# Kernel optimization log

Measured on AMD Instinct MI355X. Metric: run time of the kernel, lower is better.

Reference implementation:

```python
import jax, jax.numpy as jnp
import numpy as np

B, S, D, E, K = 4, 4096, 2048, 64, 2
LN_EPS = 1e-5
TEMP_EPS = 1e-6
Z_LOSS_COEF = 0.001
LB_COEF = 0.1


def setup_inputs() -> dict:
    key = jax.random.key(0)
    k1, k2 = jax.random.split(key)
    x = jax.random.normal(k1, (B, S, D), dtype=jnp.float32)
    # kaiming_normal fan_in (std = 1/sqrt(D)) scaled by 0.01, as in __init__
    W = jax.random.normal(k2, (E, D), dtype=jnp.float32) * jnp.float32(0.01 / np.sqrt(D))
    gamma = jnp.ones((E,), jnp.float32)   # LayerNorm weight
    beta = jnp.zeros((E,), jnp.float32)   # LayerNorm bias
    temperature = jnp.full((1,), 0.5, jnp.float32)
    return {"x": x, "W": W, "gamma": gamma, "beta": beta, "temperature": temperature}


def reference(x, W, gamma, beta, temperature):
    b, s, d = x.shape
    xf = x.reshape(-1, d)                                  # [N, D]
    logits = xf @ W.T                                      # [N, E]
    # LayerNorm over expert dim (biased variance, eps=1e-5, matches torch)
    mu = logits.mean(axis=-1, keepdims=True)
    var = jnp.mean(jnp.square(logits - mu), axis=-1, keepdims=True)
    logits = (logits - mu) * jax.lax.rsqrt(var + LN_EPS) * gamma + beta
    # temperature-scaled softmax
    routing_weights = jax.nn.softmax(logits / (temperature + TEMP_EPS), axis=-1)  # [N, E]
    # top-k + scatter into dense dispatch mask
    top_w, top_idx = jax.lax.top_k(routing_weights, K)     # [N, K]
    n = routing_weights.shape[0]
    dispatch = jnp.zeros_like(routing_weights).at[jnp.arange(n)[:, None], top_idx].set(top_w)
    dispatch = dispatch.reshape(b, s, E)                   # [B, S, E]
    # aux losses
    expert_load = dispatch.mean(axis=1)                    # [B, E]
    load_balance_loss = jnp.std(expert_load, ddof=1) / expert_load.mean() * 10.0
    router_z_loss = jnp.mean(jnp.square(logits))
    total_loss = ZLC * router_z_loss + LB_COEF * load_balance_loss if False else (
        Z_LOSS_COEF * router_z_loss + LB_COEF * load_balance_loss)
    return jax.lax.stop_gradient(routing_weights), dispatch, total_loss
```

## Files before the change

kernel.cpp:

```cpp
#include <hip/hip_runtime.h>
#include <hip/hip_bf16.h>
#include <float.h>
#include <math.h>

#define B_DIM 4
#define S_DIM 4096
#define D_DIM 2048
#define E_DIM 64
#define N_TOK 16384
#define TOKS 32
#define NBLK (N_TOK / TOKS)
#define NTHR 256
#define SLICES 4
#define DSLICE (D_DIM / SLICES)
#define KSTEPS2 16
#define GAP_THRESH 1e-3f
#define MAXFLAG 16

typedef __bf16 bf16x8_t __attribute__((ext_vector_type(8)));
typedef float f32x4_t __attribute__((ext_vector_type(4)));

union U8 { bf16x8_t v; unsigned short u[8]; };

__device__ __forceinline__ void split2(float f, unsigned short& h, unsigned short& l) {
    unsigned int u = __float_as_uint(f);
    h = (unsigned short)(u >> 16);
    float hf = __uint_as_float(u & 0xFFFF0000u);
    l = (unsigned short)(__float_as_uint(f - hf) >> 16);
}

typedef const __attribute__((address_space(1))) unsigned int* gas1_t;
typedef __attribute__((address_space(3))) unsigned int* las3_t;
__device__ __forceinline__ void gll16(const unsigned short* g, unsigned short* l) {
    __builtin_amdgcn_global_load_lds((gas1_t)(const void*)g, (las3_t)(void*)l, 16, 0, 0);
}

__global__ void wsplit(const float* __restrict__ W, unsigned short* __restrict__ wh,
                       unsigned short* __restrict__ wl, float* __restrict__ wshdr) {
    const int i = blockIdx.x * 256 + threadIdx.x;
    if (blockIdx.x == 0) { wshdr[threadIdx.x] = 0.f; wshdr[threadIdx.x + 256] = 0.f; }
    const int e    = i >> 8;
    const int k8   = i & 255;
    const int quad = k8 & 3;
    const int h    = (k8 >> 2) & 1;
    const int s    = (k8 >> 3) & 7;
    const int sl   = k8 >> 6;
    const int t    = e >> 4;
    const int l15  = e & 15;
    const int lane = quad * 16 + l15;
    const size_t f = ((size_t)((sl * 8 + s) * 2 + h) * 4 + t) * 64 + lane;
    float4 a = *(const float4*)(W + (size_t)e * D_DIM + k8 * 8);
    float4 b = *(const float4*)(W + (size_t)e * D_DIM + k8 * 8 + 4);
    ushort4 h0, l0, h1, l1;
    split2(a.x, h0.x, l0.x); split2(a.y, h0.y, l0.y);
    split2(a.z, h0.z, l0.z); split2(a.w, h0.w, l0.w);
    split2(b.x, h1.x, l1.x); split2(b.y, h1.y, l1.y);
    split2(b.z, h1.z, l1.z); split2(b.w, h1.w, l1.w);
    *(ushort4*)(wh + f * 8)     = h0;
    *(ushort4*)(wh + f * 8 + 4) = h1;
    *(ushort4*)(wl + f * 8)     = l0;
    *(ushort4*)(wl + f * 8 + 4) = l1;
}

__global__ __launch_bounds__(NTHR, 2) void router_main(
    const float* __restrict__ x, const float* __restrict__ W,
    const unsigned short* __restrict__ whg, const unsigned short* __restrict__ wlg,
    const float* __restrict__ gamma, const float* __restrict__ beta,
    const float* __restrict__ temperature,
    float* __restrict__ out_rw, float* __restrict__ out_dp,
    float* __restrict__ g_zsum, float* __restrict__ g_load)
{
    __shared__ __align__(16) unsigned char arena[65536];
    unsigned short* const bufH = (unsigned short*)arena;
    unsigned short* const bufL = (unsigned short*)(arena + 32768);
    float (* const part)[TOKS][E_DIM + 2] = (float (*)[TOKS][E_DIM + 2])arena;
    float (* const lgt)[E_DIM + 1] = (float (*)[E_DIM + 1])(arena + 33792);

    __shared__ float lgm[E_DIM], lbt[E_DIM], loadsum[E_DIM];
    __shared__ float smu[TOKS], srs[TOKS], sinv[TOKS];
    __shared__ int sel1[TOKS], sel2[TOKS];
    __shared__ int ftok[MAXFLAG], fcand[MAXFLAG][3];
    __shared__ int nflag;

    const int tid = threadIdx.x;
    const int tokBase = blockIdx.x * TOKS;
    const int lane = tid & 63;
    const int wv = tid >> 6;
    const int l15 = lane & 15;
    const int quad = lane >> 4;

    if (tid == 0) nflag = 0;
    if (tid < E_DIM) { lgm[tid] = gamma[tid]; lbt[tid] = beta[tid]; loadsum[tid] = 0.f; }

    const float* xp0 = x + (size_t)(tokBase + l15) * D_DIM      + wv * DSLICE + quad * 8;
    const float* xp1 = x + (size_t)(tokBase + 16 + l15) * D_DIM + wv * DSLICE + quad * 8;

    const unsigned short* hsrc0 = whg + (size_t)wv * 16 * 2048 + lane * 8;
    const unsigned short* lsrc0 = wlg + (size_t)wv * 16 * 2048 + lane * 8;
    unsigned short* const hdst0 = bufH + wv * 2 * 2048 + lane * 8;
    unsigned short* const ldst0 = bufL + wv * 2 * 2048 + lane * 8;

#define STAGE(S2, B) do {                                                   \
        const unsigned short* hs = hsrc0 + (size_t)(S2) * 2048;             \
        const unsigned short* ls = lsrc0 + (size_t)(S2) * 2048;             \
        unsigned short* hd = hdst0 + (B) * 2048;                            \
        unsigned short* ld = ldst0 + (B) * 2048;                            \
        gll16(hs,        hd);        gll16(ls,        ld);                  \
        gll16(hs +  512, hd +  512); gll16(ls +  512, ld +  512);           \
        gll16(hs + 1024, hd + 1024); gll16(ls + 1024, ld + 1024);           \
        gll16(hs + 1536, hd + 1536); gll16(ls + 1536, ld + 1536);           \
    } while (0)

    f32x4_t acc[2][4];
    #pragma unroll
    for (int m = 0; m < 2; ++m)
        #pragma unroll
        for (int t = 0; t < 4; ++t) acc[m][t] = (f32x4_t){0.f, 0.f, 0.f, 0.f};

    STAGE(0, 0);
    float4 xqA[4], xqB[4];
    xqA[0] = *(const float4*)(xp0);  xqA[1] = *(const float4*)(xp0 + 4);
    xqA[2] = *(const float4*)(xp1);  xqA[3] = *(const float4*)(xp1 + 4);
    asm volatile("s_waitcnt vmcnt(0)" ::: "memory");
    __builtin_amdgcn_sched_barrier(0);

    for (int s2 = 0; s2 < KSTEPS2; ++s2) {
        const int cur = s2 & 1;
        const bool more = (s2 + 1 < KSTEPS2);
        if (more) {
            STAGE(s2 + 1, cur ^ 1);
            const float* xg0 = xp0 + (s2 + 1) * 32;
            const float* xg1 = xp1 + (s2 + 1) * 32;
            xqB[0] = *(const float4*)(xg0);  xqB[1] = *(const float4*)(xg0 + 4);
            xqB[2] = *(const float4*)(xg1);  xqB[3] = *(const float4*)(xg1 + 4);
        }
        const unsigned short* hb = bufH + (wv * 2 + cur) * 2048;
        const unsigned short* lb = bufL + (wv * 2 + cur) * 2048;
        bf16x8_t bh[4], bl[4];
        #pragma unroll
        for (int t = 0; t < 4; ++t) {
            bh[t] = *(const bf16x8_t*)(hb + t * 512 + lane * 8);
            bl[t] = *(const bf16x8_t*)(lb + t * 512 + lane * 8);
        }
        #pragma unroll
        for (int m = 0; m < 2; ++m) {
            float tf[8] = {xqA[m*2].x, xqA[m*2].y, xqA[m*2].z, xqA[m*2].w,
                           xqA[m*2+1].x, xqA[m*2+1].y, xqA[m*2+1].z, xqA[m*2+1].w};
            U8 ah, al;
            #pragma unroll
            for (int k = 0; k < 8; ++k) split2(tf[k], ah.u[k], al.u[k]);
            #pragma unroll
            for (int t = 0; t < 4; ++t) {
                acc[m][t] = __builtin_amdgcn_mfma_f32_16x16x32_bf16(ah.v, bh[t], acc[m][t], 0, 0, 0);
                acc[m][t] = __builtin_amdgcn_mfma_f32_16x16x32_bf16(ah.v, bl[t], acc[m][t], 0, 0, 0);
                acc[m][t] = __builtin_amdgcn_mfma_f32_16x16x32_bf16(al.v, bh[t], acc[m][t], 0, 0, 0);
            }
        }
        if (more) {
            asm volatile("s_waitcnt vmcnt(0)" ::: "memory");
            __builtin_amdgcn_sched_barrier(0);
            #pragma unroll
            for (int j = 0; j < 4; ++j) xqA[j] = xqB[j];
        }
    }
#undef STAGE

    __syncthreads();

    #pragma unroll
    for (int m = 0; m < 2; ++m)
        #pragma unroll
        for (int t = 0; t < 4; ++t)
            #pragma unroll
            for (int r = 0; r < 4; ++r)
                part[wv][m * 16 + quad * 4 + r][t * 16 + l15] = acc[m][t][r];
    __syncthreads();

    for (int i = tid; i < TOKS * E_DIM; i += NTHR) {
        int r = i >> 6, c = i & 63;
        lgt[r][c] = (part[0][r][c] + part[1][r][c]) + (part[2][r][c] + part[3][r][c]);
    }
    __syncthreads();

    if (wv < 2) {
        const int tok = wv * 16 + l15;
        const int q = quad;
        const float it = 1.f / (temperature[0] + 1e-6f);
        float s1 = 0.f, s2 = 0.f;
        #pragma unroll
        for (int e = 0; e < 16; ++e) { float v = lgt[tok][q * 16 + e]; s1 += v; s2 += v * v; }
        s1 += __shfl_xor(s1, 16); s1 += __shfl_xor(s1, 32);
        s2 += __shfl_xor(s2, 16); s2 += __shfl_xor(s2, 32);
        const float mu  = s1 * (1.f / 64.f);
        const float var = s2 * (1.f / 64.f) - mu * mu;
        const float rs  = rsqrtf(var + 1e-5f);
        if (q == 0) { smu[tok] = mu; srs[tok] = rs; }

        float m0 = -FLT_MAX, m1 = -FLT_MAX, m2 = -FLT_MAX;
        int   i0 = -1, i1 = -1, i2 = -1;
        float zl = 0.f;
        #pragma unroll
        for (int e = 0; e < 16; ++e) {
            int c = q * 16 + e;
            float y = (lgt[tok][c] - mu) * rs * lgm[c] + lbt[c];
            lgt[tok][c] = y;
            zl += y * y;
            if (y > m0)      { m2 = m1; i2 = i1; m1 = m0; i1 = i0; m0 = y; i0 = c; }
            else if (y > m1) { m2 = m1; i2 = i1; m1 = y; i1 = c; }
            else if (y > m2) { m2 = y; i2 = c; }
        }
        #pragma unroll
        for (int d = 16; d <= 32; d <<= 1) {
            float n0 = __shfl_xor(m0, d), n1 = __shfl_xor(m1, d), n2 = __shfl_xor(m2, d);
            int   j0 = __shfl_xor(i0, d), j1 = __shfl_xor(i1, d), j2 = __shfl_xor(i2, d);
            bool t0 = (m0 > n0) || (m0 == n0 && i0 < j0);
            float r0v = t0 ? m0 : n0; int r0i = t0 ? i0 : j0;
            float A0v = t0 ? m1 : m0; int A0i = t0 ? i1 : i0;
            float A1v = t0 ? m2 : m1; int A1i = t0 ? i2 : i1;
            float B0v = t0 ? n0 : n1; int B0i = t0 ? j0 : j1;
            float B1v = t0 ? n1 : n2; int B1i = t0 ? j1 : j2;
            bool t1 = (A0v > B0v) || (A0v == B0v && A0i < B0i);
            float r1v = t1 ? A0v : B0v; int r1i = t1 ? A0i : B0i;
            float A0w = t1 ? A1v : A0v; int A0j = t1 ? A1i : A0i;
            float B0w = t1 ? B0v : B1v; int B0j = t1 ? B0i : B1i;
            bool t2 = (A0w > B0w) || (A0w == B0w && A0j < B0j);
            float r2v = t2 ? A0w : B0w; int r2i = t2 ? A0j : B0j;
            m0 = r0v; i0 = r0i; m1 = r1v; i1 = r1i; m2 = r2v; i2 = r2i;
        }
        if (q == 0) {
            sel1[tok] = i0; sel2[tok] = i1;
            if (m1 - m2 < GAP_THRESH) {
                int sf = atomicAdd(&nflag, 1);
                if (sf < MAXFLAG) { ftok[sf] = tok; fcand[sf][0] = i0; fcand[sf][1] = i1; fcand[sf][2] = i2; }
            }
        }
        float es = 0.f;
        #pragma unroll
        for (int e = 0; e < 16; ++e) {
            int c = q * 16 + e;
            float ev = __expf((lgt[tok][c] - m0) * it);
            lgt[tok][c] = ev; es += ev;
        }
        es += __shfl_xor(es, 16); es += __shfl_xor(es, 32);
        if (q == 0) sinv[tok] = 1.f / es;
        zl += __shfl_xor(zl, 1); zl += __shfl_xor(zl, 2); zl += __shfl_xor(zl, 4);
        zl += __shfl_xor(zl, 8); zl += __shfl_xor(zl, 16); zl += __shfl_xor(zl, 32);
        if (lane == 0) atomicAdd(g_zsum, zl);
    }
    __syncthreads();

    const int nf = min(nflag, MAXFLAG);
    for (int f = wv; f < nf; f += 4) {
        const int tk = ftok[f];
        const int c0 = fcand[f][0], c1 = fcand[f][1], c2 = fcand[f][2];
        const float* xr = x + (size_t)(tokBase + tk) * D_DIM;
        const float* w0 = W + (size_t)c0 * D_DIM;
        const float* w1 = W + (size_t)c1 * D_DIM;
        const float* w2 = W + (size_t)c2 * D_DIM;
        double L0 = 0.0, L1 = 0.0, L2 = 0.0;
        for (int i = lane; i < D_DIM; i += 64) {
            double xv = (double)xr[i];
            L0 += xv * (double)w0[i];
            L1 += xv * (double)w1[i];
            L2 += xv * (double)w2[i];
        }
        #pragma unroll
        for (int off = 32; off; off >>= 1) {
            L0 += __shfl_down(L0, off);
            L1 += __shfl_down(L1, off);
            L2 += __shfl_down(L2, off);
        }
        if (lane == 0) {
            double dmu = (double)smu[tk], drs = (double)srs[tk];
            double y0 = (L0 - dmu) * drs * (double)lgm[c0] + (double)lbt[c0];
            double y1 = (L1 - dmu) * drs * (double)lgm[c1] + (double)lbt[c1];
            double y2 = (L2 - dmu) * drs * (double)lgm[c2] + (double)lbt[c2];
            bool g01 = (y0 > y1) || (y0 == y1 && c0 < c1);
            bool g02 = (y0 > y2) || (y0 == y2 && c0 < c2);
            bool g12 = (y1 > y2) || (y1 == y2 && c1 < c2);
            int a, b;
            if (!g01 && !g02)      { a = c1; b = c2; }
            else if (g01 && !g12)  { a = c0; b = c2; }
            else                   { a = c0; b = c1; }
            sel1[tk] = a; sel2[tk] = b;
        }
    }
    __syncthreads();

    if (tid < TOKS) {
        float inv = sinv[tid];
        atomicAdd(&loadsum[sel1[tid]], lgt[tid][sel1[tid]] * inv);
        atomicAdd(&loadsum[sel2[tid]], lgt[tid][sel2[tid]] * inv);
    }
    __syncthreads();
    if (tid < E_DIM) atomicAdd(&g_load[(tokBase >> 12) * E_DIM + tid], loadsum[tid]);

    float* orw = out_rw + (size_t)tokBase * E_DIM;
    float* odp = out_dp + (size_t)tokBase * E_DIM;
    for (int i = tid; i < TOKS * E_DIM; i += NTHR) {
        int r = i >> 6, c = i & 63;
        float p = lgt[r][c] * sinv[r];
        orw[i] = p;
        odp[i] = (c == sel1[r] || c == sel2[r]) ? p : 0.f;
    }
}

__global__ void router_fin(const float* __restrict__ ws, float* __restrict__ out_loss) {
    __shared__ float sv[B_DIM * E_DIM];
    const int tid = threadIdx.x;
    sv[tid] = ws[8 + tid] * (1.f / S_DIM);
    __syncthreads();
    if (tid == 0) {
        float s = 0.f;
        for (int i = 0; i < B_DIM * E_DIM; ++i) s += sv[i];
        const float mean = s * (1.f / (B_DIM * E_DIM));
        float ss = 0.f;
        for (int i = 0; i < B_DIM * E_DIM; ++i) { float d = sv[i] - mean; ss += d * d; }
        const float sd = sqrtf(ss * (1.f / (B_DIM * E_DIM - 1)));
        const float z = ws[0] * (1.f / ((float)N_TOK * E_DIM));
        out_loss[0] = 0.001f * z + 0.1f * (sd / mean) * 10.f;
    }
}

extern "C" void kernel_launch(void* const* d_in, const int* in_sizes, int n_in,
                              void* d_out, int out_size, void* d_ws, size_t ws_size,
                              hipStream_t stream) {
    const float* x     = (const float*)d_in[0];
    const float* W     = (const float*)d_in[1];
    const float* gamma = (const float*)d_in[2];
    const float* beta  = (const float*)d_in[3];
    const float* temp  = (const float*)d_in[4];
    float* out  = (float*)d_out;
    float* rw   = out;
    float* dp   = out + (size_t)N_TOK * E_DIM;
    float* loss = out + 2 * (size_t)N_TOK * E_DIM;
    float* ws   = (float*)d_ws;

    unsigned short* whg = (unsigned short*)((char*)d_ws + 4096);
    unsigned short* wlg = whg + (size_t)E_DIM * D_DIM;

    wsplit<<<dim3(64), dim3(256), 0, stream>>>(W, whg, wlg, ws);
    router_main<<<dim3(NBLK), dim3(NTHR), 0, stream>>>(x, W, whg, wlg, gamma, beta, temp,
                                                       rw, dp, ws, ws + 8);
    router_fin<<<dim3(1), dim3(256), 0, stream>>>(ws, loss);
}
```

Measured before the change: 234.7 us.

## Split router into GEMM and epilogue kernels; deepen x prefetch to two stages

The fused router kernel is split in two. A GEMM kernel writes raw logits to a global workspace, and a separate epilogue kernel handles 64 tokens per block with all four waves doing LayerNorm, softmax, top-k refinement and the outputs. The GEMM loop now prefetches x two steps ahead with partial vmcnt waits, so less global-load latency sits exposed. The split adds a 4 MB round trip through global memory and one more launch, in exchange for a leaner GEMM kernel and a better-used epilogue.

```diff
diff --git a/kernel.cpp b/kernel.cpp
--- a/kernel.cpp
+++ b/kernel.cpp
@@ -14,8 +14,10 @@
 #define SLICES 4
 #define DSLICE (D_DIM / SLICES)
 #define KSTEPS2 16
+#define TOKS_E 64
+#define NBLK_E (N_TOK / TOKS_E)
 #define GAP_THRESH 1e-3f
-#define MAXFLAG 16
+#define MAXFLAG 32
 
 typedef __bf16 bf16x8_t __attribute__((ext_vector_type(8)));
 typedef float f32x4_t __attribute__((ext_vector_type(4)));
@@ -62,25 +64,15 @@
     *(ushort4*)(wl + f * 8 + 4) = l1;
 }
 
-__global__ __launch_bounds__(NTHR, 2) void router_main(
-    const float* __restrict__ x, const float* __restrict__ W,
+__global__ __launch_bounds__(NTHR, 2) void router_gemm(
+    const float* __restrict__ x,
     const unsigned short* __restrict__ whg, const unsigned short* __restrict__ wlg,
-    const float* __restrict__ gamma, const float* __restrict__ beta,
-    const float* __restrict__ temperature,
-    float* __restrict__ out_rw, float* __restrict__ out_dp,
-    float* __restrict__ g_zsum, float* __restrict__ g_load)
+    float* __restrict__ glgt)
 {
     __shared__ __align__(16) unsigned char arena[65536];
     unsigned short* const bufH = (unsigned short*)arena;
     unsigned short* const bufL = (unsigned short*)(arena + 32768);
     float (* const part)[TOKS][E_DIM + 2] = (float (*)[TOKS][E_DIM + 2])arena;
-    float (* const lgt)[E_DIM + 1] = (float (*)[E_DIM + 1])(arena + 33792);
-
-    __shared__ float lgm[E_DIM], lbt[E_DIM], loadsum[E_DIM];
-    __shared__ float smu[TOKS], srs[TOKS], sinv[TOKS];
-    __shared__ int sel1[TOKS], sel2[TOKS];
-    __shared__ int ftok[MAXFLAG], fcand[MAXFLAG][3];
-    __shared__ int nflag;
 
     const int tid = threadIdx.x;
     const int tokBase = blockIdx.x * TOKS;
@@ -88,9 +80,6 @@
     const int wv = tid >> 6;
     const int l15 = lane & 15;
     const int quad = lane >> 4;
-
-    if (tid == 0) nflag = 0;
-    if (tid < E_DIM) { lgm[tid] = gamma[tid]; lbt[tid] = beta[tid]; loadsum[tid] = 0.f; }
 
     const float* xp0 = x + (size_t)(tokBase + l15) * D_DIM      + wv * DSLICE + quad * 8;
     const float* xp1 = x + (size_t)(tokBase + 16 + l15) * D_DIM + wv * DSLICE + quad * 8;
@@ -117,22 +106,27 @@
         #pragma unroll
         for (int t = 0; t < 4; ++t) acc[m][t] = (f32x4_t){0.f, 0.f, 0.f, 0.f};
 
+    float4 xqA[4], xqB[4], xqC[4];
     STAGE(0, 0);
-    float4 xqA[4], xqB[4];
     xqA[0] = *(const float4*)(xp0);  xqA[1] = *(const float4*)(xp0 + 4);
     xqA[2] = *(const float4*)(xp1);  xqA[3] = *(const float4*)(xp1 + 4);
-    asm volatile("s_waitcnt vmcnt(0)" ::: "memory");
+    {
+        const float* xg0 = xp0 + 32;
+        const float* xg1 = xp1 + 32;
+        xqB[0] = *(const float4*)(xg0);  xqB[1] = *(const float4*)(xg0 + 4);
+        xqB[2] = *(const float4*)(xg1);  xqB[3] = *(const float4*)(xg1 + 4);
+    }
+    asm volatile("s_waitcnt vmcnt(4)" ::: "memory");
     __builtin_amdgcn_sched_barrier(0);
 
     for (int s2 = 0; s2 < KSTEPS2; ++s2) {
         const int cur = s2 & 1;
-        const bool more = (s2 + 1 < KSTEPS2);
-        if (more) {
-            STAGE(s2 + 1, cur ^ 1);
-            const float* xg0 = xp0 + (s2 + 1) * 32;
-            const float* xg1 = xp1 + (s2 + 1) * 32;
-            xqB[0] = *(const float4*)(xg0);  xqB[1] = *(const float4*)(xg0 + 4);
-            xqB[2] = *(const float4*)(xg1);  xqB[3] = *(const float4*)(xg1 + 4);
+        if (s2 + 1 < KSTEPS2) STAGE(s2 + 1, cur ^ 1);
+        if (s2 + 2 < KSTEPS2) {
+            const float* xg0 = xp0 + (s2 + 2) * 32;
+            const float* xg1 = xp1 + (s2 + 2) * 32;
+            xqC[0] = *(const float4*)(xg0);  xqC[1] = *(const float4*)(xg0 + 4);
+            xqC[2] = *(const float4*)(xg1);  xqC[3] = *(const float4*)(xg1 + 4);
         }
         const unsigned short* hb = bufH + (wv * 2 + cur) * 2048;
         const unsigned short* lb = bufL + (wv * 2 + cur) * 2048;
@@ -156,11 +150,15 @@
                 acc[m][t] = __builtin_amdgcn_mfma_f32_16x16x32_bf16(al.v, bh[t], acc[m][t], 0, 0, 0);
             }
         }
-        if (more) {
-            asm volatile("s_waitcnt vmcnt(0)" ::: "memory");
+        if (s2 + 1 < KSTEPS2) {
+            if (s2 + 2 < KSTEPS2) {
+                asm volatile("s_waitcnt vmcnt(4)" ::: "memory");
+            } else {
+                asm volatile("s_waitcnt vmcnt(0)" ::: "memory");
+            }
             __builtin_amdgcn_sched_barrier(0);
             #pragma unroll
-            for (int j = 0; j < 4; ++j) xqA[j] = xqB[j];
+            for (int j = 0; j < 4; ++j) { xqA[j] = xqB[j]; xqB[j] = xqC[j]; }
         }
     }
 #undef STAGE
@@ -176,13 +174,46 @@
                 part[wv][m * 16 + quad * 4 + r][t * 16 + l15] = acc[m][t][r];
     __syncthreads();
 
+    float* og = glgt + (size_t)tokBase * E_DIM;
     for (int i = tid; i < TOKS * E_DIM; i += NTHR) {
         int r = i >> 6, c = i & 63;
-        lgt[r][c] = (part[0][r][c] + part[1][r][c]) + (part[2][r][c] + part[3][r][c]);
-    }
-    __syncthreads();
-
-    if (wv < 2) {
+        og[i] = (part[0][r][c] + part[1][r][c]) + (part[2][r][c] + part[3][r][c]);
+    }
+}
+
+__global__ __launch_bounds__(256, 2) void router_epi(
+    const float* __restrict__ glgt, const float* __restrict__ x,
+    const float* __restrict__ W,
+    const float* __restrict__ gamma, const float* __restrict__ beta,
+    const float* __restrict__ temperature,
+    float* __restrict__ out_rw, float* __restrict__ out_dp,
+    float* __restrict__ g_zsum, float* __restrict__ g_load)
+{
+    __shared__ float lgt[TOKS_E][E_DIM + 1];
+    __shared__ float lgm[E_DIM], lbt[E_DIM], loadsum[E_DIM];
+    __shared__ float smu[TOKS_E], srs[TOKS_E], sinv[TOKS_E];
+    __shared__ int sel1[TOKS_E], sel2[TOKS_E];
+    __shared__ int ftok[MAXFLAG], fcand[MAXFLAG][3];
+    __shared__ int nflag;
+    __shared__ float zacc;
+
+    const int tid = threadIdx.x;
+    const int tokBase = blockIdx.x * TOKS_E;
+    const int lane = tid & 63;
+    const int wv = tid >> 6;
+    const int l15 = lane & 15;
+    const int quad = lane >> 4;
+
+    if (tid == 0) { nflag = 0; zacc = 0.f; }
+    if (tid < E_DIM) { lgm[tid] = gamma[tid]; lbt[tid] = beta[tid]; loadsum[tid] = 0.f; }
+    const float* ig = glgt + (size_t)tokBase * E_DIM;
+    for (int i = tid; i < TOKS_E * E_DIM; i += 256) {
+        int r = i >> 6, c = i & 63;
+        lgt[r][c] = ig[i];
+    }
+    __syncthreads();
+
+    {
         const int tok = wv * 16 + l15;
         const int q = quad;
         const float it = 1.f / (temperature[0] + 1e-6f);
@@ -245,9 +276,10 @@
         if (q == 0) sinv[tok] = 1.f / es;
         zl += __shfl_xor(zl, 1); zl += __shfl_xor(zl, 2); zl += __shfl_xor(zl, 4);
         zl += __shfl_xor(zl, 8); zl += __shfl_xor(zl, 16); zl += __shfl_xor(zl, 32);
-        if (lane == 0) atomicAdd(g_zsum, zl);
-    }
-    __syncthreads();
+        if (lane == 0) atomicAdd(&zacc, zl);
+    }
+    __syncthreads();
+    if (tid == 0) atomicAdd(g_zsum, zacc);
 
     const int nf = min(nflag, MAXFLAG);
     for (int f = wv; f < nf; f += 4) {
@@ -287,7 +319,7 @@
     }
     __syncthreads();
 
-    if (tid < TOKS) {
+    if (tid < TOKS_E) {
         float inv = sinv[tid];
         atomicAdd(&loadsum[sel1[tid]], lgt[tid][sel1[tid]] * inv);
         atomicAdd(&loadsum[sel2[tid]], lgt[tid][sel2[tid]] * inv);
@@ -297,7 +329,7 @@
 
     float* orw = out_rw + (size_t)tokBase * E_DIM;
     float* odp = out_dp + (size_t)tokBase * E_DIM;
-    for (int i = tid; i < TOKS * E_DIM; i += NTHR) {
+    for (int i = tid; i < TOKS_E * E_DIM; i += 256) {
         int r = i >> 6, c = i & 63;
         float p = lgt[r][c] * sinv[r];
         orw[i] = p;
@@ -338,9 +370,11 @@
 
     unsigned short* whg = (unsigned short*)((char*)d_ws + 4096);
     unsigned short* wlg = whg + (size_t)E_DIM * D_DIM;
+    float* glgt = (float*)((char*)d_ws + (1 << 20));
 
     wsplit<<<dim3(64), dim3(256), 0, stream>>>(W, whg, wlg, ws);
-    router_main<<<dim3(NBLK), dim3(NTHR), 0, stream>>>(x, W, whg, wlg, gamma, beta, temp,
+    router_gemm<<<dim3(NBLK), dim3(NTHR), 0, stream>>>(x, whg, wlg, glgt);
+    router_epi<<<dim3(NBLK_E), dim3(256), 0, stream>>>(glgt, x, W, gamma, beta, temp,
                                                        rw, dp, ws, ws + 8);
     router_fin<<<dim3(1), dim3(256), 0, stream>>>(ws, loss);
 }
```

Result: no change. 235.3 us (+0.3%).

## Split K across eight waves with single-buffered LDS weights and deeper x prefetch

Applied to the files above, without the earlier changes.

Blocks grow from four waves to eight, each covering a 256-wide K slice over 8 steps, so each wave's K loop is half as long. The per-wave LDS weight buffer drops from double to single buffering, and the x loads are prefetched two steps ahead using a third register set. The partial sums from the eight waves are reduced in shared memory, and the logits array gets its own allocation instead of aliasing the arena. The arena grows to about 68KB, which may reduce the number of resident blocks per CU. The single-buffered staging also depends on the waitcnt ordering being correct so that a step's reads finish before the next stage overwrites the buffer.

```diff
diff --git a/kernel.cpp b/kernel.cpp
--- a/kernel.cpp
+++ b/kernel.cpp
@@ -10,10 +10,9 @@
 #define N_TOK 16384
 #define TOKS 32
 #define NBLK (N_TOK / TOKS)
-#define NTHR 256
-#define SLICES 4
-#define DSLICE (D_DIM / SLICES)
-#define KSTEPS2 16
+#define NTHR 512
+#define WAVES 8
+#define KSTEPS 8
 #define GAP_THRESH 1e-3f
 #define MAXFLAG 16
 
@@ -62,7 +61,7 @@
     *(ushort4*)(wl + f * 8 + 4) = l1;
 }
 
-__global__ __launch_bounds__(NTHR, 2) void router_main(
+__global__ __launch_bounds__(NTHR, 4) void router_main(
     const float* __restrict__ x, const float* __restrict__ W,
     const unsigned short* __restrict__ whg, const unsigned short* __restrict__ wlg,
     const float* __restrict__ gamma, const float* __restrict__ beta,
@@ -70,12 +69,12 @@
     float* __restrict__ out_rw, float* __restrict__ out_dp,
     float* __restrict__ g_zsum, float* __restrict__ g_load)
 {
-    __shared__ __align__(16) unsigned char arena[65536];
+    __shared__ __align__(16) unsigned char arena[WAVES * TOKS * (E_DIM + 2) * 4];
     unsigned short* const bufH = (unsigned short*)arena;
     unsigned short* const bufL = (unsigned short*)(arena + 32768);
     float (* const part)[TOKS][E_DIM + 2] = (float (*)[TOKS][E_DIM + 2])arena;
-    float (* const lgt)[E_DIM + 1] = (float (*)[E_DIM + 1])(arena + 33792);
-
+
+    __shared__ float lgt[TOKS][E_DIM + 1];
     __shared__ float lgm[E_DIM], lbt[E_DIM], loadsum[E_DIM];
     __shared__ float smu[TOKS], srs[TOKS], sinv[TOKS];
     __shared__ int sel1[TOKS], sel2[TOKS];
@@ -92,23 +91,23 @@
     if (tid == 0) nflag = 0;
     if (tid < E_DIM) { lgm[tid] = gamma[tid]; lbt[tid] = beta[tid]; loadsum[tid] = 0.f; }
 
-    const float* xp0 = x + (size_t)(tokBase + l15) * D_DIM      + wv * DSLICE + quad * 8;
-    const float* xp1 = x + (size_t)(tokBase + 16 + l15) * D_DIM + wv * DSLICE + quad * 8;
-
-    const unsigned short* hsrc0 = whg + (size_t)wv * 16 * 2048 + lane * 8;
-    const unsigned short* lsrc0 = wlg + (size_t)wv * 16 * 2048 + lane * 8;
-    unsigned short* const hdst0 = bufH + wv * 2 * 2048 + lane * 8;
-    unsigned short* const ldst0 = bufL + wv * 2 * 2048 + lane * 8;
-
-#define STAGE(S2, B) do {                                                   \
-        const unsigned short* hs = hsrc0 + (size_t)(S2) * 2048;             \
-        const unsigned short* ls = lsrc0 + (size_t)(S2) * 2048;             \
-        unsigned short* hd = hdst0 + (B) * 2048;                            \
-        unsigned short* ld = ldst0 + (B) * 2048;                            \
-        gll16(hs,        hd);        gll16(ls,        ld);                  \
-        gll16(hs +  512, hd +  512); gll16(ls +  512, ld +  512);           \
-        gll16(hs + 1024, hd + 1024); gll16(ls + 1024, ld + 1024);           \
-        gll16(hs + 1536, hd + 1536); gll16(ls + 1536, ld + 1536);           \
+    const float* xp0 = x + (size_t)(tokBase + l15) * D_DIM      + wv * 256 + quad * 8;
+    const float* xp1 = x + (size_t)(tokBase + 16 + l15) * D_DIM + wv * 256 + quad * 8;
+
+    const unsigned short* hsrc0 = whg + (size_t)wv * 8 * 2048 + lane * 8;
+    const unsigned short* lsrc0 = wlg + (size_t)wv * 8 * 2048 + lane * 8;
+    unsigned short* const hdst = bufH + wv * 2048 + lane * 8;
+    unsigned short* const ldst = bufL + wv * 2048 + lane * 8;
+    const unsigned short* const hb = bufH + wv * 2048;
+    const unsigned short* const lb = bufL + wv * 2048;
+
+#define STAGE(S) do {                                                       \
+        const unsigned short* hs = hsrc0 + (size_t)(S) * 2048;              \
+        const unsigned short* ls = lsrc0 + (size_t)(S) * 2048;              \
+        gll16(hs,        hdst);        gll16(ls,        ldst);              \
+        gll16(hs +  512, hdst +  512); gll16(ls +  512, ldst +  512);       \
+        gll16(hs + 1024, hdst + 1024); gll16(ls + 1024, ldst + 1024);       \
+        gll16(hs + 1536, hdst + 1536); gll16(ls + 1536, ldst + 1536);       \
     } while (0)
 
     f32x4_t acc[2][4];
@@ -117,30 +116,32 @@
         #pragma unroll
         for (int t = 0; t < 4; ++t) acc[m][t] = (f32x4_t){0.f, 0.f, 0.f, 0.f};
 
-    STAGE(0, 0);
-    float4 xqA[4], xqB[4];
-    xqA[0] = *(const float4*)(xp0);  xqA[1] = *(const float4*)(xp0 + 4);
-    xqA[2] = *(const float4*)(xp1);  xqA[3] = *(const float4*)(xp1 + 4);
-    asm volatile("s_waitcnt vmcnt(0)" ::: "memory");
+    float4 xqA[4], xqB[4], xqC[4];
+    STAGE(0);
+    xqA[0] = *(const float4*)(xp0);      xqA[1] = *(const float4*)(xp0 + 4);
+    xqA[2] = *(const float4*)(xp1);      xqA[3] = *(const float4*)(xp1 + 4);
+    xqB[0] = *(const float4*)(xp0 + 32); xqB[1] = *(const float4*)(xp0 + 36);
+    xqB[2] = *(const float4*)(xp1 + 32); xqB[3] = *(const float4*)(xp1 + 36);
+    asm volatile("s_waitcnt vmcnt(4)" ::: "memory");
     __builtin_amdgcn_sched_barrier(0);
 
-    for (int s2 = 0; s2 < KSTEPS2; ++s2) {
-        const int cur = s2 & 1;
-        const bool more = (s2 + 1 < KSTEPS2);
-        if (more) {
-            STAGE(s2 + 1, cur ^ 1);
-            const float* xg0 = xp0 + (s2 + 1) * 32;
-            const float* xg1 = xp1 + (s2 + 1) * 32;
-            xqB[0] = *(const float4*)(xg0);  xqB[1] = *(const float4*)(xg0 + 4);
-            xqB[2] = *(const float4*)(xg1);  xqB[3] = *(const float4*)(xg1 + 4);
-        }
-        const unsigned short* hb = bufH + (wv * 2 + cur) * 2048;
-        const unsigned short* lb = bufL + (wv * 2 + cur) * 2048;
+    #pragma unroll
+    for (int s = 0; s < KSTEPS; ++s) {
         bf16x8_t bh[4], bl[4];
         #pragma unroll
         for (int t = 0; t < 4; ++t) {
             bh[t] = *(const bf16x8_t*)(hb + t * 512 + lane * 8);
             bl[t] = *(const bf16x8_t*)(lb + t * 512 + lane * 8);
+        }
+        __builtin_amdgcn_sched_barrier(0);
+        asm volatile("s_waitcnt lgkmcnt(0)" ::: "memory");
+        __builtin_amdgcn_sched_barrier(0);
+        if (s + 1 < KSTEPS) STAGE(s + 1);
+        if (s + 2 < KSTEPS) {
+            const float* xg0 = xp0 + (s + 2) * 32;
+            const float* xg1 = xp1 + (s + 2) * 32;
+            xqC[0] = *(const float4*)(xg0);  xqC[1] = *(const float4*)(xg0 + 4);
+            xqC[2] = *(const float4*)(xg1);  xqC[3] = *(const float4*)(xg1 + 4);
         }
         #pragma unroll
         for (int m = 0; m < 2; ++m) {
@@ -156,11 +157,15 @@
                 acc[m][t] = __builtin_amdgcn_mfma_f32_16x16x32_bf16(al.v, bh[t], acc[m][t], 0, 0, 0);
             }
         }
-        if (more) {
+        if (s + 2 < KSTEPS) {
+            asm volatile("s_waitcnt vmcnt(4)" ::: "memory");
+        } else if (s + 1 < KSTEPS) {
             asm volatile("s_waitcnt vmcnt(0)" ::: "memory");
-            __builtin_amdgcn_sched_barrier(0);
+        }
+        __builtin_amdgcn_sched_barrier(0);
+        if (s + 1 < KSTEPS) {
             #pragma unroll
-            for (int j = 0; j < 4; ++j) xqA[j] = xqB[j];
+            for (int j = 0; j < 4; ++j) { xqA[j] = xqB[j]; xqB[j] = xqC[j]; }
         }
     }
 #undef STAGE
@@ -178,7 +183,8 @@
 
     for (int i = tid; i < TOKS * E_DIM; i += NTHR) {
         int r = i >> 6, c = i & 63;
-        lgt[r][c] = (part[0][r][c] + part[1][r][c]) + (part[2][r][c] + part[3][r][c]);
+        lgt[r][c] = ((part[0][r][c] + part[1][r][c]) + (part[2][r][c] + part[3][r][c]))
+                  + ((part[4][r][c] + part[5][r][c]) + (part[6][r][c] + part[7][r][c]));
     }
     __syncthreads();
 
@@ -250,7 +256,7 @@
     __syncthreads();
 
     const int nf = min(nflag, MAXFLAG);
-    for (int f = wv; f < nf; f += 4) {
+    for (int f = wv; f < nf; f += 8) {
         const int tk = ftok[f];
         const int c0 = fcand[f][0], c1 = fcand[f][1], c2 = fcand[f][2];
         const float* xr = x + (size_t)(tokBase + tk) * D_DIM;
```

Result: slower. 248.6 us (+5.9%).
